# Performance work log

Measured on AMD Instinct MI355X. Metric: run time of the kernel, lower is better.

The kernel has to match this reference:

```python
import jax, jax.numpy as jnp
import numpy as np

N, E, B = 50000, 500000, 64
IN_DIM, HID, H, NC = 128, 32, 8, 10
SLOPE = 0.2  # DGL GATConv leaky_relu negative_slope default


def setup_inputs() -> dict:
    key = jax.random.key(0)
    ks = jax.random.split(key, 14)
    feat = jax.random.normal(ks[0], (N, IN_DIM), dtype=jnp.float32)
    src = jax.random.randint(ks[1], (E,), 0, N, dtype=jnp.int32)
    dst = jax.random.randint(ks[2], (E,), 0, N, dtype=jnp.int32)
    node2graph = jnp.sort(jax.random.randint(ks[3], (N,), 0, B, dtype=jnp.int32))
    s1 = 1.0 / np.sqrt(IN_DIM)
    s2 = 1.0 / np.sqrt(H * HID)
    W1 = jax.random.normal(ks[4], (IN_DIM, H * HID), dtype=jnp.float32) * s1
    al1 = jax.random.normal(ks[5], (H, HID), dtype=jnp.float32) * 0.1
    ar1 = jax.random.normal(ks[6], (H, HID), dtype=jnp.float32) * 0.1
    b1 = jnp.zeros((H * HID,), dtype=jnp.float32)
    W2 = jax.random.normal(ks[7], (H * HID, H * HID), dtype=jnp.float32) * s2
    al2 = jax.random.normal(ks[8], (H, HID), dtype=jnp.float32) * 0.1
    ar2 = jax.random.normal(ks[9], (H, HID), dtype=jnp.float32) * 0.1
    b2 = jnp.zeros((H * HID,), dtype=jnp.float32)
    Wc = jax.random.normal(ks[10], (H * HID, NC), dtype=jnp.float32) * s2
    bc = jnp.zeros((NC,), dtype=jnp.float32)
    return dict(feat=feat, src=src, dst=dst, node2graph=node2graph,
                W1=W1, al1=al1, ar1=ar1, b1=b1,
                W2=W2, al2=al2, ar2=ar2, b2=b2, Wc=Wc, bc=bc)


def gat_layer(h, src, dst, W, al, ar, b):
    # h: [N, F_in] -> out: [N, H, HID]   (DGL GATConv math, no dropout)
    fs = (h @ W).reshape(N, H, HID)                      # projected src/dst feats
    el = jnp.sum(fs * al[None], axis=-1)                 # [N, H]
    er = jnp.sum(fs * ar[None], axis=-1)                 # [N, H]
    e = jax.nn.leaky_relu(el[src] + er[dst], SLOPE)      # [E, H] per-edge logits
    # edge softmax over incoming edges of each dst node (numerically stable)
    emax = jax.ops.segment_max(e, dst, num_segments=N)   # [N, H]
    ex = jnp.exp(e - emax[dst])                          # [E, H]
    denom = jax.ops.segment_sum(ex, dst, num_segments=N) # [N, H]
    alpha = ex / denom[dst]                              # [E, H]
    msg = alpha[:, :, None] * fs[src]                    # [E, H, HID]
    rst = jax.ops.segment_sum(msg, dst, num_segments=N)  # [N, H, HID]
    return rst + b.reshape(1, H, HID)


def reference(feat, src, dst, node2graph, W1, al1, ar1, b1, W2, al2, ar2, b2, Wc, bc):
    h = jax.nn.relu(gat_layer(feat, src, dst, W1, al1, ar1, b1)).reshape(N, H * HID)
    h = gat_layer(h, src, dst, W2, al2, ar2, b2).reshape(N, H * HID)
    # dgl.mean_nodes: per-graph mean over nodes of the batched graph
    counts = jax.ops.segment_sum(jnp.ones((N,), dtype=h.dtype), node2graph, num_segments=B)
    hg = jax.ops.segment_sum(h, node2graph, num_segments=B) / jnp.maximum(counts, 1.0)[:, None]
    return hg @ Wc + bc  # [B, NC]
```

## Files before the change

### kernel.cpp

```cpp
#include <hip/hip_runtime.h>
#include <hip/hip_bf16.h>

#define N_NODES 50000
#define N_EDGES 500000
#define N_GRAPHS 64
#define FDIM 256
#define NHEAD 8
#define NC 10
#define SLOPE 0.2f
#define MPAD 50048
#define NBKT 196
#define CNTN (NBKT * 256)
#define SCAN_NB (CNTN / 1024)
#define NB1 256
#define EPB 1956
#define LDSW 40
#define PSPLIT 16
#define CAST_THREADS (256*128 + 256*256 + N_NODES)
#define CAST_NB ((CAST_THREADS + 255) / 256)

typedef __attribute__((ext_vector_type(8))) short bf16x8;
typedef __attribute__((ext_vector_type(4))) float f32x4;
typedef __attribute__((ext_vector_type(2))) float f32x2;
typedef __attribute__((ext_vector_type(4))) unsigned u32x4;

__device__ __forceinline__ unsigned short f2bf(float f) {
  unsigned x = __float_as_uint(f);
  x += 0x7fff + ((x >> 16) & 1);
  return (unsigned short)(x >> 16);
}
__device__ __forceinline__ float b2f(unsigned short u) {
  return __uint_as_float((unsigned)u << 16);
}
__device__ __forceinline__ int fswz(int node, int off) {
  return off ^ ((node & 7) << 5) ^ (((node >> 3) & 1) << 4);
}

__global__ void cast_hist_kernel(const float* __restrict__ W1, const float* __restrict__ W2,
                                 unsigned short* __restrict__ Wt1, unsigned short* __restrict__ Wt2,
                                 const int* __restrict__ n2g, int* __restrict__ gstart,
                                 const int* __restrict__ dst, int* __restrict__ counts,
                                 int* __restrict__ rowstart) {
  int t = threadIdx.x;
  if (blockIdx.x < NB1) {
    __shared__ int hist[NBKT];
    int b = blockIdx.x;
    if (t < NBKT) hist[t] = 0;
    __syncthreads();
    int start = b * EPB;
    int end = min(start + EPB, N_EDGES);
    for (int base = start + t * 4; base < end; base += 1024) {
      if (base + 3 < end) {
        int4 d = *(const int4*)(dst + base);
        atomicAdd(&hist[d.x >> 8], 1); atomicAdd(&hist[d.y >> 8], 1);
        atomicAdd(&hist[d.z >> 8], 1); atomicAdd(&hist[d.w >> 8], 1);
      } else {
        for (int e2 = base; e2 < end; ++e2) atomicAdd(&hist[dst[e2] >> 8], 1);
      }
    }
    __syncthreads();
    if (t < NBKT) counts[t * NB1 + b] = hist[t];
    return;
  }
  int e = (blockIdx.x - NB1) * 256 + t;
  if (e == 0) rowstart[N_NODES] = N_EDGES;
  if (e < 256 * 128) {
    int n = e / 128, k = e % 128;
    Wt1[(size_t)n * 128 + k] = f2bf(W1[(size_t)k * 256 + n]);
  } else if (e < 256 * 128 + 256 * 256) {
    int t2 = e - 256 * 128;
    int n = t2 / 256, k = t2 % 256;
    Wt2[(size_t)n * 256 + k] = f2bf(W2[(size_t)k * 256 + n]);
  } else {
    int i = e - (256 * 128 + 256 * 256);
    if (i < N_NODES) {
      int g1 = n2g[i];
      int g0 = (i == 0) ? -1 : n2g[i - 1];
      for (int g = g0 + 1; g <= g1; ++g) gstart[g] = i;
      if (i == N_NODES - 1) {
        for (int g = g1 + 1; g <= N_GRAPHS; ++g) gstart[g] = N_NODES;
      }
    }
  }
}

__global__ void scan_local_kernel(const int* __restrict__ deg, int* __restrict__ outv,
                                  int* __restrict__ bsum, int n) {
  __shared__ int ws[4];
  int t = threadIdx.x, lane = t & 63, w = t >> 6;
  int base = blockIdx.x * 1024 + t * 4;
  int4 v = make_int4(0, 0, 0, 0);
  if (base + 3 < n) {
    v = *(const int4*)(deg + base);
  } else {
    if (base + 0 < n) v.x = deg[base + 0];
    if (base + 1 < n) v.y = deg[base + 1];
    if (base + 2 < n) v.z = deg[base + 2];
    if (base + 3 < n) v.w = deg[base + 3];
  }
  int s = v.x + v.y + v.z + v.w;
  int x = s;
  #pragma unroll
  for (int off = 1; off < 64; off <<= 1) {
    int y = __shfl_up(x, off);
    if (lane >= off) x += y;
  }
  if (lane == 63) ws[w] = x;
  __syncthreads();
  int woff = 0;
  #pragma unroll
  for (int i = 0; i < 4; ++i) woff += (i < w) ? ws[i] : 0;
  int excl = woff + x - s;
  int4 o;
  o.x = excl;
  o.y = excl + v.x;
  o.z = excl + v.x + v.y;
  o.w = excl + v.x + v.y + v.z;
  if (base + 3 < n) {
    *(int4*)(outv + base) = o;
  } else {
    if (base + 0 < n) outv[base + 0] = o.x;
    if (base + 1 < n) outv[base + 1] = o.y;
    if (base + 2 < n) outv[base + 2] = o.z;
    if (base + 3 < n) outv[base + 3] = o.w;
  }
  if (t == 255) bsum[blockIdx.x] = woff + x;
}

__global__ void bucket_scatter_kernel(const int* __restrict__ src, const int* __restrict__ dst,
                                      const int* __restrict__ cbase, const int* __restrict__ bsum,
                                      int2* __restrict__ ebuf) {
  __shared__ int cur[NBKT];
  __shared__ int boffl[SCAN_NB];
  int t = threadIdx.x, b = blockIdx.x;
  if (t < 64) {
    int v = (t < SCAN_NB) ? bsum[t] : 0;
    int x = v;
    #pragma unroll
    for (int off = 1; off < 64; off <<= 1) {
      int y = __shfl_up(x, off);
      if (t >= off) x += y;
    }
    if (t < SCAN_NB) boffl[t] = x - v;
  }
  __syncthreads();
  if (t < NBKT) {
    int idx = t * NB1 + b;
    cur[t] = cbase[idx] + boffl[idx >> 10];
  }
  __syncthreads();
  int start = b * EPB;
  int end = min(start + EPB, N_EDGES);
  for (int base = start + t * 4; base < end; base += 1024) {
    if (base + 3 < end) {
      int4 s = *(const int4*)(src + base);
      int4 d = *(const int4*)(dst + base);
      int r;
      r = atomicAdd(&cur[d.x >> 8], 1); ebuf[r] = make_int2(s.x, d.x);
      r = atomicAdd(&cur[d.y >> 8], 1); ebuf[r] = make_int2(s.y, d.y);
      r = atomicAdd(&cur[d.z >> 8], 1); ebuf[r] = make_int2(s.z, d.z);
      r = atomicAdd(&cur[d.w >> 8], 1); ebuf[r] = make_int2(s.w, d.w);
    } else {
      for (int e2 = base; e2 < end; ++e2) {
        int dd = dst[e2];
        int r = atomicAdd(&cur[dd >> 8], 1);
        ebuf[r] = make_int2(src[e2], dd);
      }
    }
  }
}

__global__ void csr_bucket_kernel(const int2* __restrict__ ebuf, const int* __restrict__ cbase,
                                  const int* __restrict__ bsum,
                                  int* __restrict__ rowstart, int* __restrict__ esrc) {
  __shared__ int hist[256];
  __shared__ int cur[256];
  __shared__ int ws[4];
  __shared__ int boffl[SCAN_NB];
  int t = threadIdx.x;
  int bkt = blockIdx.x;
  hist[t] = 0;
  if (t >= 64 && t < 128) {
    int tt = t - 64;
    int v = (tt < SCAN_NB) ? bsum[tt] : 0;
    int x = v;
    #pragma unroll
    for (int off = 1; off < 64; off <<= 1) {
      int y = __shfl_up(x, off);
      if (tt >= off) x += y;
    }
    if (tt < SCAN_NB) boffl[tt] = x - v;
  }
  __syncthreads();
  int i0 = bkt * NB1;
  int segstart = cbase[i0] + boffl[i0 >> 10];
  int segend = N_EDGES;
  if (bkt + 1 < NBKT) {
    int i1 = (bkt + 1) * NB1;
    segend = cbase[i1] + boffl[i1 >> 10];
  }
  for (int e = segstart + t; e < segend; e += 256)
    atomicAdd(&hist[ebuf[e].y & 255], 1);
  __syncthreads();
  int lane = t & 63, w = t >> 6;
  int v = hist[t], x = v;
  #pragma unroll
  for (int off = 1; off < 64; off <<= 1) {
    int y = __shfl_up(x, off);
    if (lane >= off) x += y;
  }
  if (lane == 63) ws[w] = x;
  __syncthreads();
  int woff = 0;
  #pragma unroll
  for (int i = 0; i < 4; ++i) woff += (i < w) ? ws[i] : 0;
  int excl = woff + x - v;
  cur[t] = excl;
  int node = bkt * 256 + t;
  if (node < N_NODES) rowstart[node] = segstart + excl;
  __syncthreads();
  for (int e = segstart + t; e < segend; e += 256) {
    int2 p = ebuf[e];
    int r = atomicAdd(&cur[p.y & 255], 1);
    esrc[segstart + r] = p.x;
  }
}

template<int K, bool AF32>
__global__ void gemm_mfma(const void* __restrict__ Avoid,
                          const unsigned short* __restrict__ Wt,
                          unsigned char* __restrict__ fs,
                          const float* __restrict__ al, const float* __restrict__ ar,
                          float* __restrict__ el, float* __restrict__ er, int nrows) {
  constexpr int KC = K / 32;
  __shared__ __align__(16) unsigned short LDSbuf[(64 + 256) * LDSW];
  unsigned short* Albs = LDSbuf;
  unsigned short* Wlds = LDSbuf + 64 * LDSW;
  const float* Af = (const float*)Avoid;
  const unsigned short* Ab = (const unsigned short*)Avoid;
  int t = threadIdx.x;
  int lane = t & 63;
  int w = t >> 6;
  int row0 = blockIdx.x * 64;
  int m = lane & 15;
  int q = lane >> 4;
  float4 a32[2];
  bf16x8 a16;
  bf16x8 wtr[4];
  int arow = t >> 2, apiece = t & 3;
  int agrow = min(row0 + arow, nrows - 1);
  int frow0 = t >> 3, fquad0 = t & 7;
  int frow1 = (256 + t) >> 3, fquad1 = t & 7;
  int fgrow0 = min(row0 + frow0, nrows - 1);
  int fgrow1 = min(row0 + frow1, nrows - 1);

  auto stage = [&](int kc) {
    if (AF32) {
      a32[0] = *(const float4*)(Af + (size_t)fgrow0 * K + kc * 32 + fquad0 * 4);
      a32[1] = *(const float4*)(Af + (size_t)fgrow1 * K + kc * 32 + fquad1 * 4);
    } else {
      a16 = *(const bf16x8*)(Ab + (size_t)agrow * K + kc * 32 + apiece * 8);
    }
    #pragma unroll
    for (int j = 0; j < 4; ++j) {
      int row = j * 64 + (t >> 2);
      wtr[j] = *(const bf16x8*)(Wt + (size_t)row * K + kc * 32 + (t & 3) * 8);
    }
  };
  auto commit = [&]() {
    if (AF32) {
      ushort4 o0, o1;
      o0.x = f2bf(a32[0].x); o0.y = f2bf(a32[0].y); o0.z = f2bf(a32[0].z); o0.w = f2bf(a32[0].w);
      o1.x = f2bf(a32[1].x); o1.y = f2bf(a32[1].y); o1.z = f2bf(a32[1].z); o1.w = f2bf(a32[1].w);
      *(ushort4*)(Albs + frow0 * LDSW + fquad0 * 4) = o0;
      *(ushort4*)(Albs + frow1 * LDSW + fquad1 * 4) = o1;
    } else {
      *(bf16x8*)(Albs + arow * LDSW + apiece * 8) = a16;
    }
    #pragma unroll
    for (int j = 0; j < 4; ++j) {
      int row = j * 64 + (t >> 2);
      *(bf16x8*)(Wlds + row * LDSW + (t & 3) * 8) = wtr[j];
    }
  };

  f32x4 acc[16];
  #pragma unroll
  for (int nt = 0; nt < 16; ++nt) acc[nt] = (f32x4){0.f, 0.f, 0.f, 0.f};

  stage(0);
  commit();
  for (int kc = 0; kc < KC; ++kc) {
    __syncthreads();
    if (kc + 1 < KC) stage(kc + 1);
    bf16x8 af = *(const bf16x8*)(Albs + (w * 16 + m) * LDSW + q * 8);
    #pragma unroll
    for (int nt = 0; nt < 16; ++nt) {
      bf16x8 bfv = *(const bf16x8*)(Wlds + (nt * 16 + m) * LDSW + q * 8);
      acc[nt] = __builtin_amdgcn_mfma_f32_16x16x32_bf16(bfv, af, acc[nt], 0, 0, 0);
    }
    __syncthreads();
    if (kc + 1 < KC) commit();
  }
  unsigned char* fsst = (unsigned char*)LDSbuf;
  float* elst = (float*)(fsst + 16384);
  float* erst = elst + 512;

  int nloc = w * 16 + m;
  float elh[NHEAD], erh[NHEAD];
  #pragma unroll
  for (int h = 0; h < NHEAD; ++h) { elh[h] = 0.f; erh[h] = 0.f; }
  #pragma unroll
  for (int nt = 0; nt < 16; ++nt) {
    int h = nt >> 1;
    int c0 = (nt & 1) * 16 + q * 4;
    float4 a4 = *(const float4*)(al + h * 32 + c0);
    float4 r4 = *(const float4*)(ar + h * 32 + c0);
    elh[h] += acc[nt][0] * a4.x + acc[nt][1] * a4.y + acc[nt][2] * a4.z + acc[nt][3] * a4.w;
    erh[h] += acc[nt][0] * r4.x + acc[nt][1] * r4.y + acc[nt][2] * r4.z + acc[nt][3] * r4.w;
  }
  #pragma unroll
  for (int h = 0; h < NHEAD; ++h) {
    elh[h] += __shfl_xor(elh[h], 16); elh[h] += __shfl_xor(elh[h], 32);
    erh[h] += __shfl_xor(erh[h], 16); erh[h] += __shfl_xor(erh[h], 32);
  }
  #pragma unroll
  for (int nt = 0; nt < 16; ++nt) {
    int pk = 0;
    pk = __builtin_amdgcn_cvt_pk_fp8_f32(acc[nt][0], acc[nt][1], pk, false);
    pk = __builtin_amdgcn_cvt_pk_fp8_f32(acc[nt][2], acc[nt][3], pk, true);
    *(unsigned*)(fsst + nloc * 256 + fswz(nloc, nt * 16 + q * 4)) = (unsigned)pk;
  }
  *(float2*)(elst + nloc * 8 + q * 2) = make_float2(elh[2 * q], elh[2 * q + 1]);
  *(float2*)(erst + nloc * 8 + q * 2) = make_float2(erh[2 * q], erh[2 * q + 1]);
  __syncthreads();
  #pragma unroll
  for (int i = 0; i < 4; ++i) {
    int p = i * 4096 + t * 16;
    int nn = p >> 8, off = p & 255;
    u32x4 d = *(const u32x4*)(fsst + nn * 256 + fswz(nn, off));
    *(u32x4*)(fs + (size_t)row0 * 256 + p) = d;
  }
  if (t < 128) {
    *(float4*)(el + (size_t)row0 * 8 + t * 4) = *(const float4*)(elst + t * 4);
  } else {
    int tt = t - 128;
    *(float4*)(er + (size_t)row0 * 8 + tt * 4) = *(const float4*)(erst + tt * 4);
  }
}

template<bool RELU>
__global__ __launch_bounds__(256, 8)
void edge_agg_kernel(const int* __restrict__ rowstart, const int* __restrict__ esrc,
                     const float* __restrict__ el, const float* __restrict__ er,
                     const unsigned char* __restrict__ fs,
                     const float* __restrict__ bias,
                     unsigned short* __restrict__ out, int nnodes) {
  int gid = blockIdx.x * blockDim.x + threadIdx.x;
  int v = gid >> 6;
  int lane = threadIdx.x & 63;
  if (v >= nnodes) return;
  int h = lane >> 3;
  int t8 = lane >> 3;
  int hh = lane & 7;
  int row0 = rowstart[v];
  int deg = rowstart[v + 1] - row0;
  float er_w = er[v * NHEAD + hh];
  const unsigned char* fsl = fs + lane * 4;
  const float* elp = el;
  float4 acc0 = make_float4(0.f, 0.f, 0.f, 0.f);
  float4 acc1 = make_float4(0.f, 0.f, 0.f, 0.f);
  float ws0 = 0.f, ws1 = 0.f;

  for (int base = 0; base < deg; base += 64) {
    int mm = min(deg - base, 64);
    int es = esrc[row0 + base + min(lane, mm - 1)];
    int full = mm & ~7;
    for (int j0 = 0; j0 < full; j0 += 8) {
      int sj = __shfl(es, j0 + t8);
      float x = elp[(unsigned)sj * 8u + hh] + er_w;
      x = fmaxf(x, SLOPE * x);
      float wp = __expf(x);
      float wt[8]; unsigned f[8];
      #pragma unroll
      for (int t = 0; t < 8; ++t) {
        int s = __shfl(es, j0 + t);
        f[t] = *(const unsigned*)(fsl + ((unsigned)s << 8));
      }
      #pragma unroll
      for (int t = 0; t < 8; ++t) wt[t] = __shfl(wp, t * 8 + h);
      #pragma unroll
      for (int t = 0; t < 8; ++t) {
        float wgt = wt[t];
        f32x2 lo = __builtin_amdgcn_cvt_pk_f32_fp8(f[t], false);
        f32x2 hi = __builtin_amdgcn_cvt_pk_f32_fp8(f[t], true);
        if (t & 1) {
          ws1 += wgt;
          acc1.x = fmaf(wgt, lo.x, acc1.x);
          acc1.y = fmaf(wgt, lo.y, acc1.y);
          acc1.z = fmaf(wgt, hi.x, acc1.z);
          acc1.w = fmaf(wgt, hi.y, acc1.w);
        } else {
          ws0 += wgt;
          acc0.x = fmaf(wgt, lo.x, acc0.x);
          acc0.y = fmaf(wgt, lo.y, acc0.y);
          acc0.z = fmaf(wgt, hi.x, acc0.z);
          acc0.w = fmaf(wgt, hi.y, acc0.w);
        }
      }
    }
    if (full < mm) {
      int sj = __shfl(es, min(full + t8, mm - 1));
      float x = elp[(unsigned)sj * 8u + hh] + er_w;
      x = fmaxf(x, SLOPE * x);
      float wp = __expf(x);
      if (full + t8 >= mm) wp = 0.f;
      float wt[8]; unsigned f[8];
      #pragma unroll
      for (int t = 0; t < 8; ++t) {
        int s = __shfl(es, min(full + t, mm - 1));
        f[t] = *(const unsigned*)(fsl + ((unsigned)s << 8));
      }
      #pragma unroll
      for (int t = 0; t < 8; ++t) wt[t] = __shfl(wp, t * 8 + h);
      #pragma unroll
      for (int t = 0; t < 8; ++t) {
        float wgt = wt[t];
        f32x2 lo = __builtin_amdgcn_cvt_pk_f32_fp8(f[t], false);
        f32x2 hi = __builtin_amdgcn_cvt_pk_f32_fp8(f[t], true);
        if (t & 1) {
          ws1 += wgt;
          acc1.x = fmaf(wgt, lo.x, acc1.x);
          acc1.y = fmaf(wgt, lo.y, acc1.y);
          acc1.z = fmaf(wgt, hi.x, acc1.z);
          acc1.w = fmaf(wgt, hi.y, acc1.w);
        } else {
          ws0 += wgt;
          acc0.x = fmaf(wgt, lo.x, acc0.x);
          acc0.y = fmaf(wgt, lo.y, acc0.y);
          acc0.z = fmaf(wgt, hi.x, acc0.z);
          acc0.w = fmaf(wgt, hi.y, acc0.w);
        }
      }
    }
  }
  float wsum = ws0 + ws1;
  float4 acc;
  acc.x = acc0.x + acc1.x; acc.y = acc0.y + acc1.y;
  acc.z = acc0.z + acc1.z; acc.w = acc0.w + acc1.w;
  float rdenom = (deg > 0) ? (1.0f / wsum) : 0.f;
  const float4 b = *(const float4*)(bias + lane * 4);
  acc.x = fmaf(acc.x, rdenom, b.x);
  acc.y = fmaf(acc.y, rdenom, b.y);
  acc.z = fmaf(acc.z, rdenom, b.z);
  acc.w = fmaf(acc.w, rdenom, b.w);
  if (RELU) {
    acc.x = fmaxf(acc.x, 0.f); acc.y = fmaxf(acc.y, 0.f);
    acc.z = fmaxf(acc.z, 0.f); acc.w = fmaxf(acc.w, 0.f);
  }
  ushort4 o;
  o.x = f2bf(acc.x); o.y = f2bf(acc.y); o.z = f2bf(acc.z); o.w = f2bf(acc.w);
  *(ushort4*)(out + (size_t)v * FDIM + lane * 4) = o;
}

__global__ void pool_partial_kernel(const unsigned short* __restrict__ h2,
                                    const int* __restrict__ gstart,
                                    float* __restrict__ ppart) {
  int t = threadIdx.x;
  int g = blockIdx.x / PSPLIT;
  int s = blockIdx.x % PSPLIT;
  int n0 = gstart[g], n1 = gstart[g + 1];
  int cnt = n1 - n0;
  int chunk = (cnt + PSPLIT - 1) / PSPLIT;
  int a = n0 + s * chunk;
  int bnd = min(a + chunk, n1);
  float s0 = 0.f, s1 = 0.f, s2 = 0.f, s3 = 0.f;
  int n = a;
  for (; n + 4 <= bnd; n += 4) {
    s0 += b2f(h2[(size_t)(n + 0) * FDIM + t]);
    s1 += b2f(h2[(size_t)(n + 1) * FDIM + t]);
    s2 += b2f(h2[(size_t)(n + 2) * FDIM + t]);
    s3 += b2f(h2[(size_t)(n + 3) * FDIM + t]);
  }
  for (; n < bnd; ++n) s0 += b2f(h2[(size_t)n * FDIM + t]);
  ppart[(size_t)blockIdx.x * FDIM + t] = (s0 + s1) + (s2 + s3);
}

__global__ void pool_cls_kernel(const float* __restrict__ ppart, const int* __restrict__ gstart,
                                const float* __restrict__ Wc, const float* __restrict__ bcv,
                                float* __restrict__ out) {
  __shared__ float hgl[FDIM];
  int t = threadIdx.x, g = blockIdx.x;
  float s = 0.f;
  #pragma unroll
  for (int sp = 0; sp < PSPLIT; ++sp)
    s += ppart[(size_t)(g * PSPLIT + sp) * FDIM + t];
  hgl[t] = s;
  __syncthreads();
  int cnt = gstart[g + 1] - gstart[g];
  float inv = (cnt > 0) ? (1.0f / (float)cnt) : 1.0f;
  int w = t >> 6, lane = t & 63;
  for (int j = w; j < NC; j += 4) {
    float p = 0.f;
    #pragma unroll
    for (int k = 0; k < 4; ++k) {
      int c = lane * 4 + k;
      p += hgl[c] * Wc[c * NC + j];
    }
    #pragma unroll
    for (int off = 1; off < 64; off <<= 1) p += __shfl_xor(p, off);
    if (lane == 0) out[g * NC + j] = p * inv + bcv[j];
  }
}

extern "C" void kernel_launch(void* const* d_in, const int* in_sizes, int n_in,
                              void* d_out, int out_size, void* d_ws, size_t ws_size,
                              hipStream_t stream) {
  const float* feat = (const float*)d_in[0];
  const int* src    = (const int*)d_in[1];
  const int* dst    = (const int*)d_in[2];
  const int* n2g    = (const int*)d_in[3];
  const float* W1  = (const float*)d_in[4];
  const float* al1 = (const float*)d_in[5];
  const float* ar1 = (const float*)d_in[6];
  const float* b1  = (const float*)d_in[7];
  const float* W2  = (const float*)d_in[8];
  const float* al2 = (const float*)d_in[9];
  const float* ar2 = (const float*)d_in[10];
  const float* b2  = (const float*)d_in[11];
  const float* Wc  = (const float*)d_in[12];
  const float* bc  = (const float*)d_in[13];
  float* out = (float*)d_out;

  char* wp = (char*)d_ws;
  auto carve = [&](size_t bytes) -> void* {
    void* p = (void*)wp;
    wp += (bytes + 255) & ~(size_t)255;
    return p;
  };
  unsigned char* fs = (unsigned char*)carve((size_t)MPAD * FDIM);
  unsigned short* h1 = (unsigned short*)carve((size_t)MPAD * FDIM * 2);
  unsigned short* h2 = h1;
  unsigned short* Wt1 = (unsigned short*)carve((size_t)256 * 128 * 2);
  unsigned short* Wt2 = (unsigned short*)carve((size_t)256 * 256 * 2);
  float* el      = (float*)carve((size_t)MPAD * NHEAD * 4);
  float* er      = (float*)carve((size_t)MPAD * NHEAD * 4);
  int* rowstart  = (int*)  carve((size_t)(N_NODES + 1) * 4);
  int* esrc      = (int*)  carve((size_t)N_EDGES * 4);
  int* gstart    = (int*)  carve((size_t)(N_GRAPHS + 1) * 4);
  int* bsum      = (int*)  carve((size_t)SCAN_NB * 4);
  int* counts    = (int*)  carve((size_t)CNTN * 4);
  int* cbase     = (int*)  carve((size_t)CNTN * 4);
  int2* ebuf     = (int2*) carve((size_t)N_EDGES * 8);
  float* ppart   = (float*)carve((size_t)N_GRAPHS * PSPLIT * FDIM * 4);
  (void)ws_size; (void)n_in; (void)in_sizes; (void)out_size;

  cast_hist_kernel<<<NB1 + CAST_NB, 256, 0, stream>>>(
      W1, W2, Wt1, Wt2, n2g, gstart, dst, counts, rowstart);
  scan_local_kernel<<<SCAN_NB, 256, 0, stream>>>(counts, cbase, bsum, CNTN);
  bucket_scatter_kernel<<<NB1, 256, 0, stream>>>(src, dst, cbase, bsum, ebuf);
  csr_bucket_kernel<<<NBKT, 256, 0, stream>>>(ebuf, cbase, bsum, rowstart, esrc);

  gemm_mfma<128, true><<<MPAD / 64, 256, 0, stream>>>(
      (const void*)feat, Wt1, fs, al1, ar1, el, er, N_NODES);
  edge_agg_kernel<true><<<(N_NODES * 64 + 255) / 256, 256, 0, stream>>>(
      rowstart, esrc, el, er, fs, b1, h1, N_NODES);

  gemm_mfma<256, false><<<MPAD / 64, 256, 0, stream>>>(
      (const void*)h1, Wt2, fs, al2, ar2, el, er, N_NODES);
  edge_agg_kernel<false><<<(N_NODES * 64 + 255) / 256, 256, 0, stream>>>(
      rowstart, esrc, el, er, fs, b2, h2, N_NODES);

  pool_partial_kernel<<<N_GRAPHS * PSPLIT, 256, 0, stream>>>(h2, gstart, ppart);
  pool_cls_kernel<<<N_GRAPHS, 256, 0, stream>>>(ppart, gstart, Wc, bc, out);
}
```

Measured before the change: 214.3 us.

## Store features head-sliced and aggregate edges per head slice

Features, attention logits and hidden outputs move from node-major to head-sliced layouts, with one 32-wide fp8 slice per head and head-major el/er arrays. Edge aggregation now launches one block per (4 nodes, head), and each wavefront handles 8 edges times 8 column groups in parallel, combining them with a shuffle reduction. The intent is to shrink the gather working set per block so the slice of fs for one head stays in cache, and to load el with unit stride. The cost is 8x more blocks, each redoing the CSR and edge-index loads, and an extra cross-lane reduction. Every producer and consumer (GEMM store and A load, pooling) is changed to match.

```diff
diff --git a/kernel.cpp b/kernel.cpp
--- a/kernel.cpp
+++ b/kernel.cpp
@@ -18,6 +18,7 @@
 #define PSPLIT 16
 #define CAST_THREADS (256*128 + 256*256 + N_NODES)
 #define CAST_NB ((CAST_THREADS + 255) / 256)
+#define AGG_NB ((N_NODES / 4) * 8)
 
 typedef __attribute__((ext_vector_type(8))) short bf16x8;
 typedef __attribute__((ext_vector_type(4))) float f32x4;
@@ -259,7 +260,7 @@
       a32[0] = *(const float4*)(Af + (size_t)fgrow0 * K + kc * 32 + fquad0 * 4);
       a32[1] = *(const float4*)(Af + (size_t)fgrow1 * K + kc * 32 + fquad1 * 4);
     } else {
-      a16 = *(const bf16x8*)(Ab + (size_t)agrow * K + kc * 32 + apiece * 8);
+      a16 = *(const bf16x8*)(Ab + (size_t)kc * MPAD * 32 + (size_t)agrow * 32 + apiece * 8);
     }
     #pragma unroll
     for (int j = 0; j < 4; ++j) {
@@ -331,142 +332,99 @@
     pk = __builtin_amdgcn_cvt_pk_fp8_f32(acc[nt][2], acc[nt][3], pk, true);
     *(unsigned*)(fsst + nloc * 256 + fswz(nloc, nt * 16 + q * 4)) = (unsigned)pk;
   }
-  *(float2*)(elst + nloc * 8 + q * 2) = make_float2(elh[2 * q], elh[2 * q + 1]);
-  *(float2*)(erst + nloc * 8 + q * 2) = make_float2(erh[2 * q], erh[2 * q + 1]);
+  elst[(2 * q) * 64 + nloc] = elh[2 * q];
+  elst[(2 * q + 1) * 64 + nloc] = elh[2 * q + 1];
+  erst[(2 * q) * 64 + nloc] = erh[2 * q];
+  erst[(2 * q + 1) * 64 + nloc] = erh[2 * q + 1];
   __syncthreads();
   #pragma unroll
   for (int i = 0; i < 4; ++i) {
-    int p = i * 4096 + t * 16;
-    int nn = p >> 8, off = p & 255;
-    u32x4 d = *(const u32x4*)(fsst + nn * 256 + fswz(nn, off));
-    *(u32x4*)(fs + (size_t)row0 * 256 + p) = d;
+    int L = i * 4096 + t * 16;
+    int s = L >> 11, n = (L >> 5) & 63, c = L & 31;
+    u32x4 d = *(const u32x4*)(fsst + n * 256 + fswz(n, s * 32 + c));
+    *(u32x4*)(fs + (size_t)s * MPAD * 32 + (size_t)(row0 + n) * 32 + c) = d;
   }
   if (t < 128) {
-    *(float4*)(el + (size_t)row0 * 8 + t * 4) = *(const float4*)(elst + t * 4);
+    float4 v4 = *(const float4*)(elst + t * 4);
+    *(float4*)(el + (size_t)(t >> 4) * MPAD + row0 + ((t & 15) * 4)) = v4;
   } else {
     int tt = t - 128;
-    *(float4*)(er + (size_t)row0 * 8 + tt * 4) = *(const float4*)(erst + tt * 4);
+    float4 v4 = *(const float4*)(erst + tt * 4);
+    *(float4*)(er + (size_t)(tt >> 4) * MPAD + row0 + ((tt & 15) * 4)) = v4;
   }
 }
 
 template<bool RELU>
 __global__ __launch_bounds__(256, 8)
-void edge_agg_kernel(const int* __restrict__ rowstart, const int* __restrict__ esrc,
-                     const float* __restrict__ el, const float* __restrict__ er,
-                     const unsigned char* __restrict__ fs,
-                     const float* __restrict__ bias,
-                     unsigned short* __restrict__ out, int nnodes) {
-  int gid = blockIdx.x * blockDim.x + threadIdx.x;
-  int v = gid >> 6;
+void edge_agg_s(const int* __restrict__ rowstart, const int* __restrict__ esrc,
+                const float* __restrict__ el_t, const float* __restrict__ er_t,
+                const unsigned char* __restrict__ fs_s,
+                const float* __restrict__ bias,
+                unsigned short* __restrict__ out_s) {
+  int s = blockIdx.x & 7;
+  int w = threadIdx.x >> 6;
   int lane = threadIdx.x & 63;
-  if (v >= nnodes) return;
-  int h = lane >> 3;
-  int t8 = lane >> 3;
-  int hh = lane & 7;
+  int v = (blockIdx.x >> 3) * 4 + w;
+  int e8 = lane >> 3;
+  int c4 = lane & 7;
   int row0 = rowstart[v];
   int deg = rowstart[v + 1] - row0;
-  float er_w = er[v * NHEAD + hh];
-  const unsigned char* fsl = fs + lane * 4;
-  const float* elp = el;
-  float4 acc0 = make_float4(0.f, 0.f, 0.f, 0.f);
-  float4 acc1 = make_float4(0.f, 0.f, 0.f, 0.f);
-  float ws0 = 0.f, ws1 = 0.f;
+  float er_w = er_t[(size_t)s * MPAD + v];
+  const float* elp = el_t + (size_t)s * MPAD;
+  const unsigned char* fsp = fs_s + (size_t)s * MPAD * 32 + c4 * 4;
+  float4 acc = make_float4(0.f, 0.f, 0.f, 0.f);
+  float wsum = 0.f;
 
   for (int base = 0; base < deg; base += 64) {
     int mm = min(deg - base, 64);
     int es = esrc[row0 + base + min(lane, mm - 1)];
-    int full = mm & ~7;
-    for (int j0 = 0; j0 < full; j0 += 8) {
-      int sj = __shfl(es, j0 + t8);
-      float x = elp[(unsigned)sj * 8u + hh] + er_w;
+    for (int j0 = 0; j0 < mm; j0 += 8) {
+      int idx = j0 + e8;
+      int sj = __shfl(es, min(idx, mm - 1));
+      float x = elp[sj] + er_w;
       x = fmaxf(x, SLOPE * x);
       float wp = __expf(x);
-      float wt[8]; unsigned f[8];
-      #pragma unroll
-      for (int t = 0; t < 8; ++t) {
-        int s = __shfl(es, j0 + t);
-        f[t] = *(const unsigned*)(fsl + ((unsigned)s << 8));
-      }
-      #pragma unroll
-      for (int t = 0; t < 8; ++t) wt[t] = __shfl(wp, t * 8 + h);
-      #pragma unroll
-      for (int t = 0; t < 8; ++t) {
-        float wgt = wt[t];
-        f32x2 lo = __builtin_amdgcn_cvt_pk_f32_fp8(f[t], false);
-        f32x2 hi = __builtin_amdgcn_cvt_pk_f32_fp8(f[t], true);
-        if (t & 1) {
-          ws1 += wgt;
-          acc1.x = fmaf(wgt, lo.x, acc1.x);
-          acc1.y = fmaf(wgt, lo.y, acc1.y);
-          acc1.z = fmaf(wgt, hi.x, acc1.z);
-          acc1.w = fmaf(wgt, hi.y, acc1.w);
-        } else {
-          ws0 += wgt;
-          acc0.x = fmaf(wgt, lo.x, acc0.x);
-          acc0.y = fmaf(wgt, lo.y, acc0.y);
-          acc0.z = fmaf(wgt, hi.x, acc0.z);
-          acc0.w = fmaf(wgt, hi.y, acc0.w);
-        }
-      }
-    }
-    if (full < mm) {
-      int sj = __shfl(es, min(full + t8, mm - 1));
-      float x = elp[(unsigned)sj * 8u + hh] + er_w;
-      x = fmaxf(x, SLOPE * x);
-      float wp = __expf(x);
-      if (full + t8 >= mm) wp = 0.f;
-      float wt[8]; unsigned f[8];
-      #pragma unroll
-      for (int t = 0; t < 8; ++t) {
-        int s = __shfl(es, min(full + t, mm - 1));
-        f[t] = *(const unsigned*)(fsl + ((unsigned)s << 8));
-      }
-      #pragma unroll
-      for (int t = 0; t < 8; ++t) wt[t] = __shfl(wp, t * 8 + h);
-      #pragma unroll
-      for (int t = 0; t < 8; ++t) {
-        float wgt = wt[t];
-        f32x2 lo = __builtin_amdgcn_cvt_pk_f32_fp8(f[t], false);
-        f32x2 hi = __builtin_amdgcn_cvt_pk_f32_fp8(f[t], true);
-        if (t & 1) {
-          ws1 += wgt;
-          acc1.x = fmaf(wgt, lo.x, acc1.x);
-          acc1.y = fmaf(wgt, lo.y, acc1.y);
-          acc1.z = fmaf(wgt, hi.x, acc1.z);
-          acc1.w = fmaf(wgt, hi.y, acc1.w);
-        } else {
-          ws0 += wgt;
-          acc0.x = fmaf(wgt, lo.x, acc0.x);
-          acc0.y = fmaf(wgt, lo.y, acc0.y);
-          acc0.z = fmaf(wgt, hi.x, acc0.z);
-          acc0.w = fmaf(wgt, hi.y, acc0.w);
-        }
-      }
-    }
-  }
-  float wsum = ws0 + ws1;
-  float4 acc;
-  acc.x = acc0.x + acc1.x; acc.y = acc0.y + acc1.y;
-  acc.z = acc0.z + acc1.z; acc.w = acc0.w + acc1.w;
-  float rdenom = (deg > 0) ? (1.0f / wsum) : 0.f;
-  const float4 b = *(const float4*)(bias + lane * 4);
-  acc.x = fmaf(acc.x, rdenom, b.x);
-  acc.y = fmaf(acc.y, rdenom, b.y);
-  acc.z = fmaf(acc.z, rdenom, b.z);
-  acc.w = fmaf(acc.w, rdenom, b.w);
-  if (RELU) {
-    acc.x = fmaxf(acc.x, 0.f); acc.y = fmaxf(acc.y, 0.f);
-    acc.z = fmaxf(acc.z, 0.f); acc.w = fmaxf(acc.w, 0.f);
-  }
-  ushort4 o;
-  o.x = f2bf(acc.x); o.y = f2bf(acc.y); o.z = f2bf(acc.z); o.w = f2bf(acc.w);
-  *(ushort4*)(out + (size_t)v * FDIM + lane * 4) = o;
-}
-
-__global__ void pool_partial_kernel(const unsigned short* __restrict__ h2,
+      if (idx >= mm) wp = 0.f;
+      unsigned f = *(const unsigned*)(fsp + ((unsigned)sj << 5));
+      f32x2 lo = __builtin_amdgcn_cvt_pk_f32_fp8(f, false);
+      f32x2 hi = __builtin_amdgcn_cvt_pk_f32_fp8(f, true);
+      wsum += wp;
+      acc.x = fmaf(wp, lo.x, acc.x);
+      acc.y = fmaf(wp, lo.y, acc.y);
+      acc.z = fmaf(wp, hi.x, acc.z);
+      acc.w = fmaf(wp, hi.y, acc.w);
+    }
+  }
+  #pragma unroll
+  for (int off = 8; off < 64; off <<= 1) {
+    acc.x += __shfl_xor(acc.x, off);
+    acc.y += __shfl_xor(acc.y, off);
+    acc.z += __shfl_xor(acc.z, off);
+    acc.w += __shfl_xor(acc.w, off);
+    wsum += __shfl_xor(wsum, off);
+  }
+  if (lane < 8) {
+    float rdenom = (deg > 0) ? (1.0f / wsum) : 0.f;
+    const float4 b = *(const float4*)(bias + s * 32 + lane * 4);
+    acc.x = fmaf(acc.x, rdenom, b.x);
+    acc.y = fmaf(acc.y, rdenom, b.y);
+    acc.z = fmaf(acc.z, rdenom, b.z);
+    acc.w = fmaf(acc.w, rdenom, b.w);
+    if (RELU) {
+      acc.x = fmaxf(acc.x, 0.f); acc.y = fmaxf(acc.y, 0.f);
+      acc.z = fmaxf(acc.z, 0.f); acc.w = fmaxf(acc.w, 0.f);
+    }
+    ushort4 o;
+    o.x = f2bf(acc.x); o.y = f2bf(acc.y); o.z = f2bf(acc.z); o.w = f2bf(acc.w);
+    *(ushort4*)(out_s + (size_t)s * MPAD * 32 + (size_t)v * 32 + lane * 4) = o;
+  }
+}
+
+__global__ void pool_partial_kernel(const unsigned short* __restrict__ h2s,
                                     const int* __restrict__ gstart,
                                     float* __restrict__ ppart) {
   int t = threadIdx.x;
+  const unsigned short* hp = h2s + (size_t)(t >> 5) * MPAD * 32 + (t & 31);
   int g = blockIdx.x / PSPLIT;
   int s = blockIdx.x % PSPLIT;
   int n0 = gstart[g], n1 = gstart[g + 1];
@@ -477,12 +435,12 @@
   float s0 = 0.f, s1 = 0.f, s2 = 0.f, s3 = 0.f;
   int n = a;
   for (; n + 4 <= bnd; n += 4) {
-    s0 += b2f(h2[(size_t)(n + 0) * FDIM + t]);
-    s1 += b2f(h2[(size_t)(n + 1) * FDIM + t]);
-    s2 += b2f(h2[(size_t)(n + 2) * FDIM + t]);
-    s3 += b2f(h2[(size_t)(n + 3) * FDIM + t]);
-  }
-  for (; n < bnd; ++n) s0 += b2f(h2[(size_t)n * FDIM + t]);
+    s0 += b2f(hp[(size_t)(n + 0) * 32]);
+    s1 += b2f(hp[(size_t)(n + 1) * 32]);
+    s2 += b2f(hp[(size_t)(n + 2) * 32]);
+    s3 += b2f(hp[(size_t)(n + 3) * 32]);
+  }
+  for (; n < bnd; ++n) s0 += b2f(hp[(size_t)n * 32]);
   ppart[(size_t)blockIdx.x * FDIM + t] = (s0 + s1) + (s2 + s3);
 }
 
@@ -563,13 +521,13 @@
 
   gemm_mfma<128, true><<<MPAD / 64, 256, 0, stream>>>(
       (const void*)feat, Wt1, fs, al1, ar1, el, er, N_NODES);
-  edge_agg_kernel<true><<<(N_NODES * 64 + 255) / 256, 256, 0, stream>>>(
-      rowstart, esrc, el, er, fs, b1, h1, N_NODES);
+  edge_agg_s<true><<<AGG_NB, 256, 0, stream>>>(
+      rowstart, esrc, el, er, fs, b1, h1);
 
   gemm_mfma<256, false><<<MPAD / 64, 256, 0, stream>>>(
       (const void*)h1, Wt2, fs, al2, ar2, el, er, N_NODES);
-  edge_agg_kernel<false><<<(N_NODES * 64 + 255) / 256, 256, 0, stream>>>(
-      rowstart, esrc, el, er, fs, b2, h2, N_NODES);
+  edge_agg_s<false><<<AGG_NB, 256, 0, stream>>>(
+      rowstart, esrc, el, er, fs, b2, h2);
 
   pool_partial_kernel<<<N_GRAPHS * PSPLIT, 256, 0, stream>>>(h2, gstart, ppart);
   pool_cls_kernel<<<N_GRAPHS, 256, 0, stream>>>(ppart, gstart, Wc, bc, out);
```

After: 368.4 us. 71.9% more time.
